# Kernel optimization log

Measured on AMD Instinct MI355X. Metric: run time of the kernel, lower is better.

Reference implementation:

```python
import jax, jax.numpy as jnp
import numpy as np

DIM = 64
K = 8
B_TAIL = 3.0
HID = 128
BATCH = 131072
MIN_BIN_WIDTH = 1e-3
MIN_BIN_HEIGHT = 1e-3
MIN_DERIVATIVE = 1e-3


def setup_inputs() -> dict:
    key = jax.random.key(0)
    ks = jax.random.split(key, 9)
    nin = DIM // 2
    nout = (3 * K - 1) * (DIM - DIM // 2)
    dims = [nin, HID, HID, HID, nout]
    d = {"x": jax.random.normal(ks[0], (BATCH, DIM), jnp.float32)}
    for i in range(4):
        d[f"W{i+1}"] = jax.random.normal(ks[1 + 2 * i], (dims[i], dims[i + 1]), jnp.float32) / jnp.sqrt(dims[i])
        d[f"b{i+1}"] = jax.random.normal(ks[2 + 2 * i], (dims[i + 1],), jnp.float32) * 0.01
    return d


def _gather(a, idx):
    # a: [..., K or K+1], idx: [...] int -> [...]
    return jnp.take_along_axis(a, idx[..., None], axis=-1)[..., 0]


def _mlp(x, W1, b1, W2, b2, W3, b3, W4, b4):
    h = jax.nn.elu(x @ W1 + b1)
    h = jax.nn.elu(h @ W2 + b2)
    h = jax.nn.elu(h @ W3 + b3)
    return h @ W4 + b4


def _unconstrained_rqs_fwd(inputs, uw, uh, ud, tail_bound):
    # inputs: [B, D2]; uw/uh: [B, D2, K]; ud: [B, D2, K-1]
    num_bins = uw.shape[-1]
    left = bottom = -tail_bound
    right = top = tail_bound

    inside = (inputs >= -tail_bound) & (inputs <= tail_bound)
    x = jnp.clip(inputs, -tail_bound, tail_bound)  # safe values for spline math

    # pad derivatives and pin boundary slopes so spline matches identity tails
    const = float(np.log(np.exp(1.0 - MIN_DERIVATIVE) - 1.0))
    ud = jnp.pad(ud, [(0, 0)] * (ud.ndim - 1) + [(1, 1)], constant_values=const)

    widths = jax.nn.softmax(uw, axis=-1)
    widths = MIN_BIN_WIDTH + (1.0 - MIN_BIN_WIDTH * num_bins) * widths
    cumwidths = jnp.cumsum(widths, axis=-1)
    cumwidths = jnp.pad(cumwidths, [(0, 0)] * (cumwidths.ndim - 1) + [(1, 0)])
    cumwidths = (right - left) * cumwidths + left
    cumwidths = cumwidths.at[..., 0].set(left).at[..., -1].set(right)
    widths = cumwidths[..., 1:] - cumwidths[..., :-1]

    derivatives = MIN_DERIVATIVE + jax.nn.softplus(ud)

    heights = jax.nn.softmax(uh, axis=-1)
    heights = MIN_BIN_HEIGHT + (1.0 - MIN_BIN_HEIGHT * num_bins) * heights
    cumheights = jnp.cumsum(heights, axis=-1)
    cumheights = jnp.pad(cumheights, [(0, 0)] * (cumheights.ndim - 1) + [(1, 0)])
    cumheights = (top - bottom) * cumheights + bottom
    cumheights = cumheights.at[..., 0].set(bottom).at[..., -1].set(top)
    heights = cumheights[..., 1:] - cumheights[..., :-1]

    # searchsorted: number of bin edges <= x, minus one (eps on last edge)
    cw = cumwidths.at[..., -1].add(1e-6)
    bin_idx = jnp.sum((x[..., None] >= cw).astype(jnp.int32), axis=-1) - 1
    bin_idx = jnp.clip(bin_idx, 0, num_bins - 1)

    in_cw = _gather(cumwidths, bin_idx)
    in_w = _gather(widths, bin_idx)
    in_ch = _gather(cumheights, bin_idx)
    in_h = _gather(heights, bin_idx)
    delta = heights / widths
    in_delta = _gather(delta, bin_idx)
    in_d = _gather(derivatives, bin_idx)
    in_d1 = _gather(derivatives[..., 1:], bin_idx)

    theta = (x - in_cw) / in_w
    t1mt = theta * (1.0 - theta)
    numerator = in_h * (in_delta * theta ** 2 + in_d * t1mt)
    denominator = in_delta + (in_d + in_d1 - 2.0 * in_delta) * t1mt
    spline_out = in_ch + numerator / denominator
    deriv_num = in_delta ** 2 * (in_d1 * theta ** 2 + 2.0 * in_delta * t1mt + in_d * (1.0 - theta) ** 2)
    spline_ld = jnp.log(deriv_num) - 2.0 * jnp.log(denominator)

    outputs = jnp.where(inside, spline_out, inputs)
    logabsdet = jnp.where(inside, spline_ld, 0.0)
    return outputs, logabsdet


def reference(x, W1, b1, W2, b2, W3, b3, W4, b4):
    d_half = DIM // 2
    x1, x2 = x[:, :d_half], x[:, d_half:]
    out = _mlp(x1, W1, b1, W2, b2, W3, b3, W4, b4)
    out = out.reshape(-1, DIM - d_half, 3 * K - 1)
    W = out[..., :K]
    H = out[..., K:2 * K]
    D = out[..., 2 * K:]
    y2, ld = _unconstrained_rqs_fwd(x2, W, H, D, B_TAIL)
    log_det = jnp.sum(ld, axis=1)
    return jnp.concatenate([x1, y2], axis=1), log_det
```

## Files before the change

kernel.cpp:

```cpp
#include <hip/hip_runtime.h>
#include <hip/hip_bf16.h>
#include <math.h>

typedef _Float16 f16_t;
typedef _Float16 f16x8 __attribute__((ext_vector_type(8)));
typedef float f32x4 __attribute__((ext_vector_type(4)));

#define BATCH 131072
#define MTILE 64
#define NBLK (BATCH / MTILE)

#define W1F 0
#define W2F 4096
#define W3F 20480
#define W4F 36864

__global__ __launch_bounds__(256) void convert_weights_kernel(
    const float* __restrict__ W1, const float* __restrict__ W2,
    const float* __restrict__ W3, const float* __restrict__ W4,
    f16_t* __restrict__ wf) {
  int tid = blockIdx.x * 256 + threadIdx.x;
  if (tid >= 16896) return;
  int lane = tid & 63;
  int l16 = lane & 15, lhi = lane >> 4;
  const float* W; int ncols, col, k0; bool zero = false;
  if (tid < 512) {
    int n = tid >> 6;
    W = W1; ncols = 128; col = n * 16 + l16; k0 = lhi * 8;
  } else if (tid < 2560) {
    int g = tid - 512; int n = g >> 8, s = (g >> 6) & 3;
    W = W2; ncols = 128; col = n * 16 + l16; k0 = s * 32 + lhi * 8;
  } else if (tid < 4608) {
    int g = tid - 2560; int n = g >> 8, s = (g >> 6) & 3;
    W = W3; ncols = 128; col = n * 16 + l16; k0 = s * 32 + lhi * 8;
  } else {
    int g = tid - 4608; int t = g >> 8, s = (g >> 6) & 3;
    int c = t / 6, n = t - c * 6;
    int colc = n * 16 + l16;
    W = W4; ncols = 736; col = c * 92 + colc; k0 = s * 32 + lhi * 8;
    zero = (colc >= 92);
  }
  f16x8 v;
#pragma unroll
  for (int j = 0; j < 8; ++j)
    v[j] = zero ? (f16_t)0.f : (f16_t)W[(k0 + j) * ncols + col];
  *(f16x8*)(wf + (size_t)tid * 8) = v;
}

__device__ __forceinline__ void mid_layer_ip(f16_t* hH,
                                             const f16_t* __restrict__ wseg,
                                             const float* __restrict__ bg,
                                             int wv, int l16, int lhi, int lane) {
  f16x8 a[4];
#pragma unroll
  for (int s = 0; s < 4; ++s)
    a[s] = *(const f16x8*)&hH[(wv * 16 + l16) * 136 + s * 32 + lhi * 8];
#pragma unroll
  for (int n = 0; n < 8; ++n) {
    f32x4 acc = {0.f, 0.f, 0.f, 0.f};
#pragma unroll
    for (int s = 0; s < 4; ++s) {
      f16x8 b = *(const f16x8*)(wseg + (size_t)((n * 4 + s) * 64 + lane) * 8);
      acc = __builtin_amdgcn_mfma_f32_16x16x32_f16(a[s], b, acc, 0, 0, 0);
    }
    float bias = bg[n * 16 + l16];
#pragma unroll
    for (int r = 0; r < 4; ++r) {
      float v = acc[r] + bias;
      v = v > 0.f ? v : (__expf(v) - 1.f);
      hH[(wv * 16 + lhi * 4 + r) * 136 + n * 16 + l16] = (f16_t)v;
    }
  }
}

__global__ __launch_bounds__(256, 3) void nsf_fused_kernel(
    const float* __restrict__ x,
    const float* __restrict__ b1g, const float* __restrict__ b2g,
    const float* __restrict__ b3g, const float* __restrict__ b4g,
    const f16_t* __restrict__ wf,
    float* __restrict__ out) {
  __shared__ f16_t hH[64 * 136];
  __shared__ float prm[64 * 100];
  __shared__ float x2s[64 * 33];

  const int tid = threadIdx.x;
  const int lane = tid & 63;
  const int wv = tid >> 6;
  const int l16 = lane & 15, lhi = lane >> 4;
  const int row0 = blockIdx.x * MTILE;

  {
    const float4* x4 = (const float4*)(x + (size_t)row0 * 64);
    float4* o4 = (float4*)(out + (size_t)row0 * 64);
#pragma unroll
    for (int it = 0; it < 4; ++it) {
      int idx = tid + it * 256;
      int row = idx >> 4, q = idx & 15;
      float4 v = x4[row * 16 + q];
      if (q < 8) {
        o4[row * 16 + q] = v;
        f16_t* p = &hH[row * 136 + q * 4];
        p[0] = (f16_t)v.x; p[1] = (f16_t)v.y;
        p[2] = (f16_t)v.z; p[3] = (f16_t)v.w;
      } else {
        int cb = row * 33 + (q - 8) * 4;
        x2s[cb + 0] = v.x; x2s[cb + 1] = v.y;
        x2s[cb + 2] = v.z; x2s[cb + 3] = v.w;
      }
    }
  }
  __syncthreads();

  {
    f16x8 a = *(const f16x8*)&hH[(wv * 16 + l16) * 136 + lhi * 8];
#pragma unroll
    for (int n = 0; n < 8; ++n) {
      f16x8 b = *(const f16x8*)(wf + W1F + (size_t)(n * 64 + lane) * 8);
      f32x4 acc = {0.f, 0.f, 0.f, 0.f};
      acc = __builtin_amdgcn_mfma_f32_16x16x32_f16(a, b, acc, 0, 0, 0);
      float bias = b1g[n * 16 + l16];
#pragma unroll
      for (int r = 0; r < 4; ++r) {
        float v = acc[r] + bias;
        v = v > 0.f ? v : (__expf(v) - 1.f);
        hH[(wv * 16 + lhi * 4 + r) * 136 + n * 16 + l16] = (f16_t)v;
      }
    }
  }

  mid_layer_ip(hH, wf + W2F, b2g, wv, l16, lhi, lane);
  mid_layer_ip(hH, wf + W3F, b3g, wv, l16, lhi, lane);

  {
    f16x8 a4[4];
#pragma unroll
    for (int s = 0; s < 4; ++s)
      a4[s] = *(const f16x8*)&hH[(wv * 16 + l16) * 136 + s * 32 + lhi * 8];

    const int srow = tid >> 2;
    const int sjj = tid & 3;
    float ldp = 0.f;

    for (int c = 0; c < 8; ++c) {
#pragma unroll
      for (int n = 0; n < 6; ++n) {
        f32x4 acc = {0.f, 0.f, 0.f, 0.f};
#pragma unroll
        for (int s = 0; s < 4; ++s) {
          f16x8 b = *(const f16x8*)(wf + W4F +
                      (size_t)(((c * 6 + n) * 4 + s) * 64 + lane) * 8);
          acc = __builtin_amdgcn_mfma_f32_16x16x32_f16(a4[s], b, acc, 0, 0, 0);
        }
        int colc = n * 16 + l16;
        if (colc < 92) {
          float bias = b4g[c * 92 + colc];
#pragma unroll
          for (int r = 0; r < 4; ++r)
            prm[(wv * 16 + lhi * 4 + r) * 100 + colc] = acc[r] + bias;
        }
      }
      __syncthreads();

      {
        const float* P = &prm[srow * 100 + sjj * 23];
        float uw[8], uh[8], ud[7];
#pragma unroll
        for (int i = 0; i < 8; ++i) uw[i] = P[i];
#pragma unroll
        for (int i = 0; i < 8; ++i) uh[i] = P[8 + i];
#pragma unroll
        for (int i = 0; i < 7; ++i) ud[i] = P[16 + i];

        float mw = uw[0];
#pragma unroll
        for (int i = 1; i < 8; ++i) mw = fmaxf(mw, uw[i]);
        float ew[8], sw = 0.f;
#pragma unroll
        for (int i = 0; i < 8; ++i) { ew[i] = __expf(uw[i] - mw); sw += ew[i]; }
        float invw = 1.f / sw;
        float cw[9]; cw[0] = -3.f;
        float accw = 0.f;
#pragma unroll
        for (int i = 0; i < 8; ++i) {
          accw += 0.001f + 0.992f * ew[i] * invw;
          cw[i + 1] = -3.f + 6.f * accw;
        }
        cw[8] = 3.f;
        float wd[8];
#pragma unroll
        for (int i = 0; i < 8; ++i) wd[i] = cw[i + 1] - cw[i];

        float mh = uh[0];
#pragma unroll
        for (int i = 1; i < 8; ++i) mh = fmaxf(mh, uh[i]);
        float eh[8], sh = 0.f;
#pragma unroll
        for (int i = 0; i < 8; ++i) { eh[i] = __expf(uh[i] - mh); sh += eh[i]; }
        float invh = 1.f / sh;
        float ch[9]; ch[0] = -3.f;
        float acch = 0.f;
#pragma unroll
        for (int i = 0; i < 8; ++i) {
          acch += 0.001f + 0.992f * eh[i] * invh;
          ch[i + 1] = -3.f + 6.f * acch;
        }
        ch[8] = 3.f;
        float ht[8];
#pragma unroll
        for (int i = 0; i < 8; ++i) ht[i] = ch[i + 1] - ch[i];

        float dd[9]; dd[0] = 1.f; dd[8] = 1.f;
#pragma unroll
        for (int i = 0; i < 7; ++i) {
          float u = ud[i];
          float sp = fmaxf(u, 0.f) + __logf(1.f + __expf(-fabsf(u)));
          dd[i + 1] = 0.001f + sp;
        }

        int jg = c * 4 + sjj;
        float xv = x2s[srow * 33 + jg];
        float xc = fminf(fmaxf(xv, -3.f), 3.f);

        int bin = 0;
#pragma unroll
        for (int i = 1; i < 8; ++i) bin += (xc >= cw[i]) ? 1 : 0;

        float in_cw = cw[0], in_w = wd[0], in_ch = ch[0], in_h = ht[0];
        float in_d = dd[0], in_d1 = dd[1];
#pragma unroll
        for (int i = 1; i < 8; ++i) {
          bool g = (bin >= i);
          in_cw = g ? cw[i] : in_cw;  in_w = g ? wd[i] : in_w;
          in_ch = g ? ch[i] : in_ch;  in_h = g ? ht[i] : in_h;
          in_d  = g ? dd[i] : in_d;   in_d1 = g ? dd[i + 1] : in_d1;
        }

        float dlt = in_h / in_w;
        float th = (xc - in_cw) / in_w;
        float om = 1.f - th;
        float t1 = th * om;
        float num = in_h * (dlt * th * th + in_d * t1);
        float den = dlt + (in_d + in_d1 - 2.f * dlt) * t1;
        float yo = in_ch + num / den;
        float dn = dlt * dlt * (in_d1 * th * th + 2.f * dlt * t1 + in_d * om * om);
        float ldv = __logf(dn / (den * den));
        bool inside = (xv >= -3.f) && (xv <= 3.f);
        out[(size_t)(row0 + srow) * 64 + 32 + jg] = inside ? yo : xv;
        ldp += inside ? ldv : 0.f;
      }
      __syncthreads();
    }

    float tot = ldp;
    tot += __shfl_xor(tot, 1, 64);
    tot += __shfl_xor(tot, 2, 64);
    if ((tid & 3) == 0)
      out[(size_t)BATCH * 64 + row0 + srow] = tot;
  }
}

extern "C" void kernel_launch(void* const* d_in, const int* in_sizes, int n_in,
                              void* d_out, int out_size, void* d_ws, size_t ws_size,
                              hipStream_t stream) {
  const float* x  = (const float*)d_in[0];
  const float* W1 = (const float*)d_in[1];
  const float* b1 = (const float*)d_in[2];
  const float* W2 = (const float*)d_in[3];
  const float* b2 = (const float*)d_in[4];
  const float* W3 = (const float*)d_in[5];
  const float* b3 = (const float*)d_in[6];
  const float* W4 = (const float*)d_in[7];
  const float* b4 = (const float*)d_in[8];
  f16_t* wf = (f16_t*)d_ws;
  float* out = (float*)d_out;

  hipLaunchKernelGGL(convert_weights_kernel, dim3(66), dim3(256), 0, stream,
                     W1, W2, W3, W4, wf);
  hipLaunchKernelGGL(nsf_fused_kernel, dim3(NBLK), dim3(256), 0, stream,
                     x, b1, b2, b3, b4, wf, out);
}
```

Baseline: 112.9 us.

## Make each wave own 32 rows independently with wave barriers and fp16 params

Each wave now handles 32 rows, issuing two MFMAs per weight fragment so every global B-fragment load is reused twice, and the block tile grows to 128 rows. Block-wide __syncthreads are replaced by wave barriers because each wave only touches its own slice of shared memory. The spline parameter staging buffer is now fp16, aliased onto the hidden-activation buffer, and the x2 staging copy is dropped in favour of re-reading x from global memory. Shared memory drops enough to target 4 blocks per CU, at the cost of fp16 rounding of spline logits and more registers per wave.

```diff
diff --git a/kernel.cpp b/kernel.cpp
--- a/kernel.cpp
+++ b/kernel.cpp
@@ -7,7 +7,8 @@
 typedef float f32x4 __attribute__((ext_vector_type(4)));
 
 #define BATCH 131072
-#define MTILE 64
+#define RPW 32
+#define MTILE 128
 #define NBLK (BATCH / MTILE)
 
 #define W1F 0
@@ -47,215 +48,243 @@
   *(f16x8*)(wf + (size_t)tid * 8) = v;
 }
 
-__device__ __forceinline__ void mid_layer_ip(f16_t* hH,
-                                             const f16_t* __restrict__ wseg,
-                                             const float* __restrict__ bg,
-                                             int wv, int l16, int lhi, int lane) {
-  f16x8 a[4];
-#pragma unroll
-  for (int s = 0; s < 4; ++s)
-    a[s] = *(const f16x8*)&hH[(wv * 16 + l16) * 136 + s * 32 + lhi * 8];
+__device__ __forceinline__ float elu(float v) {
+  return v > 0.f ? v : (__expf(v) - 1.f);
+}
+
+__device__ __forceinline__ void rqs_task(const f16_t* P, float xv,
+                                         float& yout, float& ldout) {
+  f16x8 pw = *(const f16x8*)P;
+  f16x8 ph = *(const f16x8*)(P + 8);
+  f16x8 pd = *(const f16x8*)(P + 16);
+  float uw[8], uh[8], ud7[7];
+#pragma unroll
+  for (int i = 0; i < 8; ++i) uw[i] = (float)pw[i];
+#pragma unroll
+  for (int i = 0; i < 8; ++i) uh[i] = (float)ph[i];
+#pragma unroll
+  for (int i = 0; i < 7; ++i) ud7[i] = (float)pd[i];
+
+  float mw = uw[0];
+#pragma unroll
+  for (int i = 1; i < 8; ++i) mw = fmaxf(mw, uw[i]);
+  float ew[8], sw = 0.f;
+#pragma unroll
+  for (int i = 0; i < 8; ++i) { ew[i] = __expf(uw[i] - mw); sw += ew[i]; }
+  float invw = 1.f / sw;
+  float cw[9]; cw[0] = -3.f;
+  float accw = 0.f;
+#pragma unroll
+  for (int i = 0; i < 8; ++i) {
+    accw += 0.001f + 0.992f * ew[i] * invw;
+    cw[i + 1] = -3.f + 6.f * accw;
+  }
+  cw[8] = 3.f;
+  float wd[8];
+#pragma unroll
+  for (int i = 0; i < 8; ++i) wd[i] = cw[i + 1] - cw[i];
+
+  float mh = uh[0];
+#pragma unroll
+  for (int i = 1; i < 8; ++i) mh = fmaxf(mh, uh[i]);
+  float eh[8], sh = 0.f;
+#pragma unroll
+  for (int i = 0; i < 8; ++i) { eh[i] = __expf(uh[i] - mh); sh += eh[i]; }
+  float invh = 1.f / sh;
+  float ch[9]; ch[0] = -3.f;
+  float acch = 0.f;
+#pragma unroll
+  for (int i = 0; i < 8; ++i) {
+    acch += 0.001f + 0.992f * eh[i] * invh;
+    ch[i + 1] = -3.f + 6.f * acch;
+  }
+  ch[8] = 3.f;
+  float ht[8];
+#pragma unroll
+  for (int i = 0; i < 8; ++i) ht[i] = ch[i + 1] - ch[i];
+
+  float dd[9]; dd[0] = 1.f; dd[8] = 1.f;
+#pragma unroll
+  for (int i = 0; i < 7; ++i) {
+    float u = ud7[i];
+    float sp = fmaxf(u, 0.f) + __logf(1.f + __expf(-fabsf(u)));
+    dd[i + 1] = 0.001f + sp;
+  }
+
+  float xc = fminf(fmaxf(xv, -3.f), 3.f);
+  int bin = 0;
+#pragma unroll
+  for (int i = 1; i < 8; ++i) bin += (xc >= cw[i]) ? 1 : 0;
+
+  float in_cw = cw[0], in_w = wd[0], in_ch = ch[0], in_h = ht[0];
+  float in_d = dd[0], in_d1 = dd[1];
+#pragma unroll
+  for (int i = 1; i < 8; ++i) {
+    bool g = (bin >= i);
+    in_cw = g ? cw[i] : in_cw;  in_w = g ? wd[i] : in_w;
+    in_ch = g ? ch[i] : in_ch;  in_h = g ? ht[i] : in_h;
+    in_d  = g ? dd[i] : in_d;   in_d1 = g ? dd[i + 1] : in_d1;
+  }
+
+  float dlt = in_h / in_w;
+  float th = (xc - in_cw) / in_w;
+  float om = 1.f - th;
+  float t1 = th * om;
+  float num = in_h * (dlt * th * th + in_d * t1);
+  float den = dlt + (in_d + in_d1 - 2.f * dlt) * t1;
+  float yo = in_ch + num / den;
+  float dn = dlt * dlt * (in_d1 * th * th + 2.f * dlt * t1 + in_d * om * om);
+  float ldv = __logf(dn / (den * den));
+  bool inside = (xv >= -3.f) && (xv <= 3.f);
+  yout = inside ? yo : xv;
+  ldout = inside ? ldv : 0.f;
+}
+
+__device__ __forceinline__ void mid_layer2(f16_t* hW,
+                                           const f16_t* __restrict__ wseg,
+                                           const float* __restrict__ bg,
+                                           int l16, int lhi, int lane) {
+  f16x8 a0[4], a1[4];
+#pragma unroll
+  for (int s = 0; s < 4; ++s) {
+    a0[s] = *(const f16x8*)&hW[l16 * 136 + s * 32 + lhi * 8];
+    a1[s] = *(const f16x8*)&hW[(16 + l16) * 136 + s * 32 + lhi * 8];
+  }
 #pragma unroll
   for (int n = 0; n < 8; ++n) {
-    f32x4 acc = {0.f, 0.f, 0.f, 0.f};
+    f32x4 c0 = {0.f, 0.f, 0.f, 0.f}, c1 = {0.f, 0.f, 0.f, 0.f};
 #pragma unroll
     for (int s = 0; s < 4; ++s) {
       f16x8 b = *(const f16x8*)(wseg + (size_t)((n * 4 + s) * 64 + lane) * 8);
-      acc = __builtin_amdgcn_mfma_f32_16x16x32_f16(a[s], b, acc, 0, 0, 0);
+      c0 = __builtin_amdgcn_mfma_f32_16x16x32_f16(a0[s], b, c0, 0, 0, 0);
+      c1 = __builtin_amdgcn_mfma_f32_16x16x32_f16(a1[s], b, c1, 0, 0, 0);
     }
     float bias = bg[n * 16 + l16];
 #pragma unroll
     for (int r = 0; r < 4; ++r) {
-      float v = acc[r] + bias;
-      v = v > 0.f ? v : (__expf(v) - 1.f);
-      hH[(wv * 16 + lhi * 4 + r) * 136 + n * 16 + l16] = (f16_t)v;
-    }
-  }
-}
-
-__global__ __launch_bounds__(256, 3) void nsf_fused_kernel(
+      hW[(lhi * 4 + r) * 136 + n * 16 + l16]      = (f16_t)elu(c0[r] + bias);
+      hW[(16 + lhi * 4 + r) * 136 + n * 16 + l16] = (f16_t)elu(c1[r] + bias);
+    }
+  }
+}
+
+__global__ __launch_bounds__(256, 4) void nsf_fused_kernel(
     const float* __restrict__ x,
     const float* __restrict__ b1g, const float* __restrict__ b2g,
     const float* __restrict__ b3g, const float* __restrict__ b4g,
     const f16_t* __restrict__ wf,
     float* __restrict__ out) {
-  __shared__ f16_t hH[64 * 136];
-  __shared__ float prm[64 * 100];
-  __shared__ float x2s[64 * 33];
+  __shared__ f16_t hH[MTILE * 136];
 
   const int tid = threadIdx.x;
   const int lane = tid & 63;
   const int wv = tid >> 6;
   const int l16 = lane & 15, lhi = lane >> 4;
-  const int row0 = blockIdx.x * MTILE;
+  const int row0 = blockIdx.x * MTILE + wv * RPW;
+  f16_t* hW = hH + wv * RPW * 136;
 
   {
     const float4* x4 = (const float4*)(x + (size_t)row0 * 64);
     float4* o4 = (float4*)(out + (size_t)row0 * 64);
 #pragma unroll
-    for (int it = 0; it < 4; ++it) {
-      int idx = tid + it * 256;
-      int row = idx >> 4, q = idx & 15;
-      float4 v = x4[row * 16 + q];
-      if (q < 8) {
-        o4[row * 16 + q] = v;
-        f16_t* p = &hH[row * 136 + q * 4];
-        p[0] = (f16_t)v.x; p[1] = (f16_t)v.y;
-        p[2] = (f16_t)v.z; p[3] = (f16_t)v.w;
-      } else {
-        int cb = row * 33 + (q - 8) * 4;
-        x2s[cb + 0] = v.x; x2s[cb + 1] = v.y;
-        x2s[cb + 2] = v.z; x2s[cb + 3] = v.w;
-      }
-    }
-  }
-  __syncthreads();
+    for (int i = 0; i < 4; ++i) {
+      int flat = i * 64 + lane;
+      int r = flat >> 3, f = flat & 7;
+      float4 v = x4[r * 16 + f];
+      o4[r * 16 + f] = v;
+      f16_t* p = &hW[r * 136 + f * 4];
+      p[0] = (f16_t)v.x; p[1] = (f16_t)v.y;
+      p[2] = (f16_t)v.z; p[3] = (f16_t)v.w;
+    }
+  }
+  __builtin_amdgcn_wave_barrier();
 
   {
-    f16x8 a = *(const f16x8*)&hH[(wv * 16 + l16) * 136 + lhi * 8];
+    f16x8 a0 = *(const f16x8*)&hW[l16 * 136 + lhi * 8];
+    f16x8 a1 = *(const f16x8*)&hW[(16 + l16) * 136 + lhi * 8];
 #pragma unroll
     for (int n = 0; n < 8; ++n) {
       f16x8 b = *(const f16x8*)(wf + W1F + (size_t)(n * 64 + lane) * 8);
-      f32x4 acc = {0.f, 0.f, 0.f, 0.f};
-      acc = __builtin_amdgcn_mfma_f32_16x16x32_f16(a, b, acc, 0, 0, 0);
+      f32x4 c0 = {0.f, 0.f, 0.f, 0.f}, c1 = {0.f, 0.f, 0.f, 0.f};
+      c0 = __builtin_amdgcn_mfma_f32_16x16x32_f16(a0, b, c0, 0, 0, 0);
+      c1 = __builtin_amdgcn_mfma_f32_16x16x32_f16(a1, b, c1, 0, 0, 0);
       float bias = b1g[n * 16 + l16];
 #pragma unroll
       for (int r = 0; r < 4; ++r) {
-        float v = acc[r] + bias;
-        v = v > 0.f ? v : (__expf(v) - 1.f);
-        hH[(wv * 16 + lhi * 4 + r) * 136 + n * 16 + l16] = (f16_t)v;
+        hW[(lhi * 4 + r) * 136 + n * 16 + l16]      = (f16_t)elu(c0[r] + bias);
+        hW[(16 + lhi * 4 + r) * 136 + n * 16 + l16] = (f16_t)elu(c1[r] + bias);
       }
     }
   }
-
-  mid_layer_ip(hH, wf + W2F, b2g, wv, l16, lhi, lane);
-  mid_layer_ip(hH, wf + W3F, b3g, wv, l16, lhi, lane);
+  __builtin_amdgcn_wave_barrier();
+
+  mid_layer2(hW, wf + W2F, b2g, l16, lhi, lane);
+  __builtin_amdgcn_wave_barrier();
+  mid_layer2(hW, wf + W3F, b3g, l16, lhi, lane);
+  __builtin_amdgcn_wave_barrier();
 
   {
-    f16x8 a4[4];
-#pragma unroll
-    for (int s = 0; s < 4; ++s)
-      a4[s] = *(const f16x8*)&hH[(wv * 16 + l16) * 136 + s * 32 + lhi * 8];
-
-    const int srow = tid >> 2;
-    const int sjj = tid & 3;
-    float ldp = 0.f;
+    f16x8 a40[4], a41[4];
+#pragma unroll
+    for (int s = 0; s < 4; ++s) {
+      a40[s] = *(const f16x8*)&hW[l16 * 136 + s * 32 + lhi * 8];
+      a41[s] = *(const f16x8*)&hW[(16 + l16) * 136 + s * 32 + lhi * 8];
+    }
+    __builtin_amdgcn_wave_barrier();
+
+    f16_t* prW = hW;
+    float ldp0 = 0.f, ldp1 = 0.f;
 
     for (int c = 0; c < 8; ++c) {
 #pragma unroll
       for (int n = 0; n < 6; ++n) {
-        f32x4 acc = {0.f, 0.f, 0.f, 0.f};
+        f32x4 c0 = {0.f, 0.f, 0.f, 0.f}, c1 = {0.f, 0.f, 0.f, 0.f};
 #pragma unroll
         for (int s = 0; s < 4; ++s) {
           f16x8 b = *(const f16x8*)(wf + W4F +
                       (size_t)(((c * 6 + n) * 4 + s) * 64 + lane) * 8);
-          acc = __builtin_amdgcn_mfma_f32_16x16x32_f16(a4[s], b, acc, 0, 0, 0);
+          c0 = __builtin_amdgcn_mfma_f32_16x16x32_f16(a40[s], b, c0, 0, 0, 0);
+          c1 = __builtin_amdgcn_mfma_f32_16x16x32_f16(a41[s], b, c1, 0, 0, 0);
         }
         int colc = n * 16 + l16;
         if (colc < 92) {
+          int dim = (colc * 90) >> 11;
+          int j = colc - dim * 23;
           float bias = b4g[c * 92 + colc];
 #pragma unroll
-          for (int r = 0; r < 4; ++r)
-            prm[(wv * 16 + lhi * 4 + r) * 100 + colc] = acc[r] + bias;
+          for (int r = 0; r < 4; ++r) {
+            prW[((lhi * 4 + r) * 4 + dim) * 24 + j]        = (f16_t)(c0[r] + bias);
+            prW[((16 + lhi * 4 + r) * 4 + dim) * 24 + j]   = (f16_t)(c1[r] + bias);
+          }
         }
       }
-      __syncthreads();
+      __builtin_amdgcn_wave_barrier();
 
       {
-        const float* P = &prm[srow * 100 + sjj * 23];
-        float uw[8], uh[8], ud[7];
-#pragma unroll
-        for (int i = 0; i < 8; ++i) uw[i] = P[i];
-#pragma unroll
-        for (int i = 0; i < 8; ++i) uh[i] = P[8 + i];
-#pragma unroll
-        for (int i = 0; i < 7; ++i) ud[i] = P[16 + i];
-
-        float mw = uw[0];
-#pragma unroll
-        for (int i = 1; i < 8; ++i) mw = fmaxf(mw, uw[i]);
-        float ew[8], sw = 0.f;
-#pragma unroll
-        for (int i = 0; i < 8; ++i) { ew[i] = __expf(uw[i] - mw); sw += ew[i]; }
-        float invw = 1.f / sw;
-        float cw[9]; cw[0] = -3.f;
-        float accw = 0.f;
-#pragma unroll
-        for (int i = 0; i < 8; ++i) {
-          accw += 0.001f + 0.992f * ew[i] * invw;
-          cw[i + 1] = -3.f + 6.f * accw;
-        }
-        cw[8] = 3.f;
-        float wd[8];
-#pragma unroll
-        for (int i = 0; i < 8; ++i) wd[i] = cw[i + 1] - cw[i];
-
-        float mh = uh[0];
-#pragma unroll
-        for (int i = 1; i < 8; ++i) mh = fmaxf(mh, uh[i]);
-        float eh[8], sh = 0.f;
-#pragma unroll
-        for (int i = 0; i < 8; ++i) { eh[i] = __expf(uh[i] - mh); sh += eh[i]; }
-        float invh = 1.f / sh;
-        float ch[9]; ch[0] = -3.f;
-        float acch = 0.f;
-#pragma unroll
-        for (int i = 0; i < 8; ++i) {
-          acch += 0.001f + 0.992f * eh[i] * invh;
-          ch[i + 1] = -3.f + 6.f * acch;
-        }
-        ch[8] = 3.f;
-        float ht[8];
-#pragma unroll
-        for (int i = 0; i < 8; ++i) ht[i] = ch[i + 1] - ch[i];
-
-        float dd[9]; dd[0] = 1.f; dd[8] = 1.f;
-#pragma unroll
-        for (int i = 0; i < 7; ++i) {
-          float u = ud[i];
-          float sp = fmaxf(u, 0.f) + __logf(1.f + __expf(-fabsf(u)));
-          dd[i + 1] = 0.001f + sp;
-        }
-
-        int jg = c * 4 + sjj;
-        float xv = x2s[srow * 33 + jg];
-        float xc = fminf(fmaxf(xv, -3.f), 3.f);
-
-        int bin = 0;
-#pragma unroll
-        for (int i = 1; i < 8; ++i) bin += (xc >= cw[i]) ? 1 : 0;
-
-        float in_cw = cw[0], in_w = wd[0], in_ch = ch[0], in_h = ht[0];
-        float in_d = dd[0], in_d1 = dd[1];
-#pragma unroll
-        for (int i = 1; i < 8; ++i) {
-          bool g = (bin >= i);
-          in_cw = g ? cw[i] : in_cw;  in_w = g ? wd[i] : in_w;
-          in_ch = g ? ch[i] : in_ch;  in_h = g ? ht[i] : in_h;
-          in_d  = g ? dd[i] : in_d;   in_d1 = g ? dd[i + 1] : in_d1;
-        }
-
-        float dlt = in_h / in_w;
-        float th = (xc - in_cw) / in_w;
-        float om = 1.f - th;
-        float t1 = th * om;
-        float num = in_h * (dlt * th * th + in_d * t1);
-        float den = dlt + (in_d + in_d1 - 2.f * dlt) * t1;
-        float yo = in_ch + num / den;
-        float dn = dlt * dlt * (in_d1 * th * th + 2.f * dlt * t1 + in_d * om * om);
-        float ldv = __logf(dn / (den * den));
-        bool inside = (xv >= -3.f) && (xv <= 3.f);
-        out[(size_t)(row0 + srow) * 64 + 32 + jg] = inside ? yo : xv;
-        ldp += inside ? ldv : 0.f;
+        int rl = lane >> 2, dim = lane & 3;
+        int jg = c * 4 + dim;
+        float y0, l0, y1, l1;
+        float xv0 = x[(size_t)(row0 + rl) * 64 + 32 + jg];
+        rqs_task(prW + (rl * 4 + dim) * 24, xv0, y0, l0);
+        out[(size_t)(row0 + rl) * 64 + 32 + jg] = y0;
+        ldp0 += l0;
+        float xv1 = x[(size_t)(row0 + rl + 16) * 64 + 32 + jg];
+        rqs_task(prW + ((rl + 16) * 4 + dim) * 24, xv1, y1, l1);
+        out[(size_t)(row0 + rl + 16) * 64 + 32 + jg] = y1;
+        ldp1 += l1;
       }
-      __syncthreads();
-    }
-
-    float tot = ldp;
-    tot += __shfl_xor(tot, 1, 64);
-    tot += __shfl_xor(tot, 2, 64);
-    if ((tid & 3) == 0)
-      out[(size_t)BATCH * 64 + row0 + srow] = tot;
+      __builtin_amdgcn_wave_barrier();
+    }
+
+    ldp0 += __shfl_xor(ldp0, 1, 64);
+    ldp0 += __shfl_xor(ldp0, 2, 64);
+    ldp1 += __shfl_xor(ldp1, 1, 64);
+    ldp1 += __shfl_xor(ldp1, 2, 64);
+    if ((lane & 3) == 0) {
+      float* ldo = out + (size_t)BATCH * 64;
+      ldo[row0 + (lane >> 2)] = ldp0;
+      ldo[row0 + (lane >> 2) + 16] = ldp1;
+    }
   }
 }
 
```

Result: slower. 151.5 us (+34.2%).
